# Kernel tuning notes

Measured on AMD Instinct MI355X. Metric: run time of the kernel, lower is better.

## Reference

```python
import jax, jax.numpy as jnp
import numpy as np

N, D, C = 4096, 512, 64
MARGIN = 1.0
INF = jnp.float32(1e30)


def setup_inputs() -> dict:
    key = jax.random.key(0)
    k1, k2 = jax.random.split(key)
    embeddings = jax.random.normal(k1, (N, D), dtype=jnp.float32)
    targets = jax.random.randint(k2, (N,), 0, C)
    return {"embeddings": embeddings, "targets": targets}


def _triplet_loss(embeddings, targets, margin=MARGIN):
    # Squared pairwise distances [N, N] (differentiable, used for the loss)
    sq_norms = jnp.sum(embeddings * embeddings, axis=1)
    sq_dist = jnp.maximum(
        sq_norms[:, None] + sq_norms[None, :] - 2.0 * (embeddings @ embeddings.T), 0.0
    )
    # Euclidean distances for mining only (index selection is non-differentiable in torch)
    dist = jnp.sqrt(jax.lax.stop_gradient(sq_dist))

    same = targets[:, None] == targets[None, :]  # [N, N] same-label mask

    # Hardest negative per anchor: argmax_k (d_ap - d_ak + margin) == argmin_k d_ak over negatives
    neg_dist = jnp.where(same, INF, dist)
    n_idx = jnp.argmin(neg_dist, axis=1)   # [N] hardest negative index per anchor
    min_neg = jnp.min(neg_dist, axis=1)    # [N] its euclidean distance

    idx = jnp.arange(dist.shape[0])
    # anchor-positive pairs: same label, a < p (torch.combinations on sorted indices)
    pair_mask = same & (idx[:, None] < idx[None, :])
    # triplet kept only if mined loss (euclidean) strictly positive
    valid = pair_mask & (dist - min_neg[:, None] + margin > 0)

    ap_sq = sq_dist                         # [N, N] squared anchor-positive distances
    an_sq = sq_dist[idx, n_idx]             # [N]   squared anchor-hard-negative distances
    losses = jax.nn.relu(ap_sq - an_sq[:, None] + margin)

    cnt = jnp.sum(valid)
    denom = jnp.maximum(cnt, 1).astype(losses.dtype)
    loss = jnp.sum(jnp.where(valid, losses, 0.0)) / denom

    correct = jnp.sum(valid & (ap_sq < an_sq[:, None]))
    accuracy = correct.astype(jnp.float32) / jnp.maximum(cnt, 1).astype(jnp.float32)
    return loss, accuracy


def reference(embeddings, targets):
    return _triplet_loss(embeddings, targets)
```

## Files before the change

kernel.cpp:

```cpp
#include <hip/hip_runtime.h>

#define N 4096
#define D 512
#define C 64
#define MARGIN 1.0f
#define TILE 64
#define ROWB 128
#define NTILES (N / TILE)
#define NTRI (NTILES * (NTILES + 1) / 2)
#define FINF 3.0e38f
#define SLOTW 16
#define PCAP 512
#define LOSSB 128

typedef __attribute__((ext_vector_type(8))) short short8;
typedef __attribute__((ext_vector_type(4))) float floatx4;

__device__ __forceinline__ unsigned short f2bf(float f) {
  unsigned int u = __float_as_uint(f);
  u += 0x7FFFu + ((u >> 16) & 1u);
  return (unsigned short)(u >> 16);
}

__device__ __forceinline__ void gload_lds16(const void* g, void* l) {
  __builtin_amdgcn_global_load_lds(
      (const __attribute__((address_space(1))) unsigned int*)g,
      (__attribute__((address_space(3))) unsigned int*)l, 16, 0, 0);
}

__global__ __launch_bounds__(256) void prep_kernel(const float* __restrict__ E,
                                                   unsigned short* __restrict__ Ebf,
                                                   float* __restrict__ norms,
                                                   unsigned int* __restrict__ an_sq_bits,
                                                   unsigned int* __restrict__ accs_u,
                                                   unsigned int* __restrict__ ctrl) {
  const int row = blockIdx.x;
  const int tid = threadIdx.x;
  if (row == N) {
    for (int k = tid; k < C * SLOTW; k += 256) accs_u[k] = 0u;
    if (tid < 2) ctrl[tid] = 0u;
    return;
  }
  if (row < 16) an_sq_bits[row * 256 + tid] = 0x7F800000u;
  const float2 v = reinterpret_cast<const float2*>(E + (size_t)row * D)[tid];
  float s = v.x * v.x + v.y * v.y;
  unsigned int packed = ((unsigned int)f2bf(v.y) << 16) | (unsigned int)f2bf(v.x);
  reinterpret_cast<unsigned int*>(Ebf + (size_t)row * D)[tid] = packed;
  for (int off = 32; off > 0; off >>= 1) s += __shfl_down(s, off);
  __shared__ float wsum[4];
  if ((tid & 63) == 0) wsum[tid >> 6] = s;
  __syncthreads();
  if (tid == 0) norms[row] = wsum[0] + wsum[1] + wsum[2] + wsum[3];
}

__global__ __launch_bounds__(256, 4) void gemm_min_kernel(const unsigned short* __restrict__ Ebf,
                                                          const float* __restrict__ norms,
                                                          const int* __restrict__ targets,
                                                          unsigned int* __restrict__ an_sq_bits,
                                                          uint2* __restrict__ pairs,
                                                          unsigned int* __restrict__ ctrl) {
  const int u = (blockIdx.x & 7) * (NTRI / 8) + (blockIdx.x >> 3);
  int i = (int)((sqrtf(8.0f * (float)u + 1.0f) - 1.0f) * 0.5f);
  while ((i + 1) * (i + 2) / 2 <= u) ++i;
  while (i * (i + 1) / 2 > u) --i;
  const int tm = u - i * (i + 1) / 2;
  const int tn = i;

  __shared__ alignas(16) unsigned char As[TILE * ROWB];
  __shared__ alignas(16) unsigned char Bs[TILE * ROWB];
  __shared__ float s_rmin[2][TILE];
  __shared__ float s_cmin[2][TILE];
  __shared__ unsigned int s_pkey[PCAP];
  __shared__ float s_psq[PCAP];
  __shared__ unsigned int s_pcnt, s_pbase;

  const int tid = threadIdx.x;
  const int wave = tid >> 6, lane = tid & 63;
  const int quad = lane >> 4, l16 = lane & 15;
  const int wr = wave >> 1, wc = wave & 1;
  const int rowBase = tm * TILE, colBase = tn * TILE;
  if (tid == 0) s_pcnt = 0u;

  const int lr = lane >> 3;
  const int lq = (lane & 7) ^ lr;
  const int lofs = lr * (D * 2) + lq * 16;
  const unsigned char* gA = (const unsigned char*)Ebf + (size_t)rowBase * (D * 2);
  const unsigned char* gB = (const unsigned char*)Ebf + (size_t)colBase * (D * 2);

  const int swz = l16 & 7;
  int rA[2], rB[2], cq[2];
#pragma unroll
  for (int s = 0; s < 2; s++) {
    rA[s] = (wr * 32 + s * 16 + l16) * ROWB;
    rB[s] = (wc * 32 + s * 16 + l16) * ROWB;
  }
#pragma unroll
  for (int ks = 0; ks < 2; ks++) cq[ks] = ((ks * 4 + quad) ^ swz) * 16;

  floatx4 acc[2][2];
#pragma unroll
  for (int a = 0; a < 2; a++)
#pragma unroll
    for (int b = 0; b < 2; b++) acc[a][b] = (floatx4){0.f, 0.f, 0.f, 0.f};

  for (int k0b = 0; k0b < D * 2; k0b += 128) {
#pragma unroll
    for (int t = 0; t < 2; t++) {
      const int g = wave * 2 + t;
      gload_lds16(gA + (size_t)g * 8 * (D * 2) + lofs + k0b, As + g * 1024);
      gload_lds16(gB + (size_t)g * 8 * (D * 2) + lofs + k0b, Bs + g * 1024);
    }
    __syncthreads();
#pragma unroll
    for (int ks = 0; ks < 2; ks++) {
      short8 af[2], bf[2];
#pragma unroll
      for (int s = 0; s < 2; s++) {
        af[s] = *reinterpret_cast<const short8*>(As + rA[s] + cq[ks]);
        bf[s] = *reinterpret_cast<const short8*>(Bs + rB[s] + cq[ks]);
      }
#pragma unroll
      for (int sm = 0; sm < 2; sm++)
#pragma unroll
        for (int sn = 0; sn < 2; sn++)
          acc[sm][sn] = __builtin_amdgcn_mfma_f32_16x16x32_bf16(af[sm], bf[sn], acc[sm][sn], 0, 0, 0);
    }
    __syncthreads();
  }

  int tcol[2], gcolv[2];
  float ncol[2];
#pragma unroll
  for (int sn = 0; sn < 2; sn++) {
    const int gc = colBase + wc * 32 + sn * 16 + l16;
    gcolv[sn] = gc;
    tcol[sn] = targets[gc];
    ncol[sn] = norms[gc];
  }
  float colmin[2] = {FINF, FINF};
#pragma unroll
  for (int sm = 0; sm < 2; sm++) {
#pragma unroll
    for (int r = 0; r < 4; r++) {
      const int rloc = wr * 32 + sm * 16 + quad * 4 + r;
      const int grow = rowBase + rloc;
      const int trow = targets[grow];
      const float nrow = norms[grow];
      float rowmin = FINF;
#pragma unroll
      for (int sn = 0; sn < 2; sn++) {
        const float sq = fmaxf(nrow + ncol[sn] - 2.0f * acc[sm][sn][r], 0.0f);
        if (tcol[sn] != trow) {
          rowmin = fminf(rowmin, sq);
          colmin[sn] = fminf(colmin[sn], sq);
        } else if (grow < gcolv[sn]) {
          const unsigned int idx = atomicAdd(&s_pcnt, 1u);
          if (idx < PCAP) {
            s_pkey[idx] = ((unsigned int)grow << 12) | (unsigned int)gcolv[sn];
            s_psq[idx] = sq;
          } else {
            const unsigned int g = atomicAdd(&ctrl[0], 1u);
            pairs[g] = make_uint2(((unsigned int)grow << 12) | (unsigned int)gcolv[sn],
                                  __float_as_uint(sq));
          }
        }
      }
#pragma unroll
      for (int off = 1; off < 16; off <<= 1) rowmin = fminf(rowmin, __shfl_xor(rowmin, off));
      if (l16 == 0) s_rmin[wc][rloc] = rowmin;
    }
  }
#pragma unroll
  for (int sn = 0; sn < 2; sn++) {
    float cm = colmin[sn];
    cm = fminf(cm, __shfl_xor(cm, 16));
    cm = fminf(cm, __shfl_xor(cm, 32));
    if (quad == 0) s_cmin[wr][wc * 32 + sn * 16 + l16] = cm;
  }
  __syncthreads();
  if (tid < TILE) {
    const float m = fminf(s_rmin[0][tid], s_rmin[1][tid]);
    if (m < FINF) atomicMin(&an_sq_bits[rowBase + tid], __float_as_uint(m));
  } else if (tid < 2 * TILE) {
    const int c = tid - TILE;
    const float m = fminf(s_cmin[0][c], s_cmin[1][c]);
    if (m < FINF) atomicMin(&an_sq_bits[colBase + c], __float_as_uint(m));
  }
  const unsigned int npair = min(s_pcnt, (unsigned int)PCAP);
  if (tid == 0) s_pbase = atomicAdd(&ctrl[0], npair);
  __syncthreads();
  for (unsigned int r = tid; r < npair; r += 256)
    pairs[s_pbase + r] = make_uint2(s_pkey[r], __float_as_uint(s_psq[r]));
}

__global__ __launch_bounds__(256) void loss_kernel(const uint2* __restrict__ pairs,
                                                   const unsigned int* __restrict__ an_sq_bits,
                                                   float* __restrict__ accs,
                                                   unsigned int* __restrict__ ctrl,
                                                   float* __restrict__ out) {
  const int tid = threadIdx.x, wave = tid >> 6, lane = tid & 63;
  const unsigned int M = ctrl[0];
  __shared__ float s_sum[4];
  __shared__ unsigned int s_cnt[4], s_cor[4];
  __shared__ int s_last;
  float bsum = 0.f;
  unsigned int bcnt = 0, bcor = 0;
  for (unsigned int r = blockIdx.x * 256 + tid; r < M; r += LOSSB * 256) {
    const uint2 rec = pairs[r];
    const int a = (int)(rec.x >> 12);
    const float sq = __uint_as_float(rec.y);
    const float an = __uint_as_float(an_sq_bits[a]);
    if (sqrtf(sq) - sqrtf(an) + MARGIN > 0.0f) {
      bcnt++;
      bsum += fmaxf(sq - an + MARGIN, 0.0f);
      if (sq < an) bcor++;
    }
  }
#pragma unroll
  for (int off = 32; off > 0; off >>= 1) {
    bsum += __shfl_down(bsum, off);
    bcnt += __shfl_down(bcnt, off);
    bcor += __shfl_down(bcor, off);
  }
  if (lane == 0) { s_sum[wave] = bsum; s_cnt[wave] = bcnt; s_cor[wave] = bcor; }
  __syncthreads();
  if (tid == 0) {
    float* slot = accs + (size_t)(blockIdx.x & (C - 1)) * SLOTW;
    atomicAdd(&slot[0], s_sum[0] + s_sum[1] + s_sum[2] + s_sum[3]);
    atomicAdd((unsigned int*)&slot[1], s_cnt[0] + s_cnt[1] + s_cnt[2] + s_cnt[3]);
    atomicAdd((unsigned int*)&slot[2], s_cor[0] + s_cor[1] + s_cor[2] + s_cor[3]);
    __threadfence();
    s_last = (atomicAdd(&ctrl[1], 1u) == (unsigned int)LOSSB - 1u);
  }
  __syncthreads();
  if (s_last) {
    __threadfence();
    if (tid < C) {
      float sum = __uint_as_float(atomicAdd((unsigned int*)&accs[(size_t)tid * SLOTW + 0], 0u));
      unsigned int cnt = atomicAdd((unsigned int*)&accs[(size_t)tid * SLOTW + 1], 0u);
      unsigned int cor = atomicAdd((unsigned int*)&accs[(size_t)tid * SLOTW + 2], 0u);
#pragma unroll
      for (int off = 32; off > 0; off >>= 1) {
        sum += __shfl_down(sum, off);
        cnt += __shfl_down(cnt, off);
        cor += __shfl_down(cor, off);
      }
      if (tid == 0) {
        const float denom = (float)(cnt > 0u ? cnt : 1u);
        out[0] = sum / denom;
        out[1] = (float)cor / denom;
      }
    }
  }
}

extern "C" void kernel_launch(void* const* d_in, const int* in_sizes, int n_in,
                              void* d_out, int out_size, void* d_ws, size_t ws_size,
                              hipStream_t stream) {
  const float* E = (const float*)d_in[0];
  const int* targets = (const int*)d_in[1];
  float* out = (float*)d_out;
  char* ws = (char*)d_ws;
  size_t off = 0;
  unsigned short* Ebf = (unsigned short*)(ws + off); off += (size_t)N * D * 2;
  float* norms = (float*)(ws + off); off += (size_t)N * 4;
  unsigned int* an_sq = (unsigned int*)(ws + off); off += (size_t)N * 4;
  float* accs = (float*)(ws + off); off += (size_t)C * SLOTW * 4;
  unsigned int* ctrl = (unsigned int*)(ws + off); off += 256;
  uint2* pairs = (uint2*)(ws + off);

  prep_kernel<<<dim3(N + 1), dim3(256), 0, stream>>>(E, Ebf, norms, an_sq, (unsigned int*)accs, ctrl);
  gemm_min_kernel<<<dim3(NTRI), dim3(256), 0, stream>>>(Ebf, norms, targets, an_sq, pairs, ctrl);
  loss_kernel<<<dim3(LOSSB), dim3(256), 0, stream>>>(pairs, an_sq, accs, ctrl, out);
}
```

Baseline: 110.1 us.

## Pre-layout bf16 embeddings in MFMA fragment order and load operands directly from global

The prep kernel now writes the bf16 embeddings in a blocked layout matching the 16x16x32 MFMA operand fragment order, with 16-row groups and 1KB chunks along K. The GEMM kernel drops the LDS staging buffers, the global-to-LDS loads and both barriers, and has each wave read its fragments straight from global memory with 16-byte loads. This removes LDS traffic and synchronisation and frees shared memory. The cost is that A and B tiles are no longer shared through LDS within a block, so each wave fetches them again and relies on L1/L2 hits.

Result: slower. 121.0 us (+9.9%).

```diff
diff --git a/kernel.cpp b/kernel.cpp
--- a/kernel.cpp
+++ b/kernel.cpp
@@ -5,7 +5,6 @@
 #define C 64
 #define MARGIN 1.0f
 #define TILE 64
-#define ROWB 128
 #define NTILES (N / TILE)
 #define NTRI (NTILES * (NTILES + 1) / 2)
 #define FINF 3.0e38f
@@ -22,14 +21,8 @@
   return (unsigned short)(u >> 16);
 }
 
-__device__ __forceinline__ void gload_lds16(const void* g, void* l) {
-  __builtin_amdgcn_global_load_lds(
-      (const __attribute__((address_space(1))) unsigned int*)g,
-      (__attribute__((address_space(3))) unsigned int*)l, 16, 0, 0);
-}
-
 __global__ __launch_bounds__(256) void prep_kernel(const float* __restrict__ E,
-                                                   unsigned short* __restrict__ Ebf,
+                                                   unsigned int* __restrict__ Ebt,
                                                    float* __restrict__ norms,
                                                    unsigned int* __restrict__ an_sq_bits,
                                                    unsigned int* __restrict__ accs_u,
@@ -45,7 +38,7 @@
   const float2 v = reinterpret_cast<const float2*>(E + (size_t)row * D)[tid];
   float s = v.x * v.x + v.y * v.y;
   unsigned int packed = ((unsigned int)f2bf(v.y) << 16) | (unsigned int)f2bf(v.x);
-  reinterpret_cast<unsigned int*>(Ebf + (size_t)row * D)[tid] = packed;
+  Ebt[((size_t)(row >> 4) << 12) + ((tid >> 4) << 8) + ((row & 15) << 4) + (tid & 15)] = packed;
   for (int off = 32; off > 0; off >>= 1) s += __shfl_down(s, off);
   __shared__ float wsum[4];
   if ((tid & 63) == 0) wsum[tid >> 6] = s;
@@ -53,7 +46,7 @@
   if (tid == 0) norms[row] = wsum[0] + wsum[1] + wsum[2] + wsum[3];
 }
 
-__global__ __launch_bounds__(256, 4) void gemm_min_kernel(const unsigned short* __restrict__ Ebf,
+__global__ __launch_bounds__(256, 4) void gemm_min_kernel(const unsigned int* __restrict__ Ebt,
                                                           const float* __restrict__ norms,
                                                           const int* __restrict__ targets,
                                                           unsigned int* __restrict__ an_sq_bits,
@@ -66,8 +59,6 @@
   const int tm = u - i * (i + 1) / 2;
   const int tn = i;
 
-  __shared__ alignas(16) unsigned char As[TILE * ROWB];
-  __shared__ alignas(16) unsigned char Bs[TILE * ROWB];
   __shared__ float s_rmin[2][TILE];
   __shared__ float s_cmin[2][TILE];
   __shared__ unsigned int s_pkey[PCAP];
@@ -81,21 +72,15 @@
   const int rowBase = tm * TILE, colBase = tn * TILE;
   if (tid == 0) s_pcnt = 0u;
 
-  const int lr = lane >> 3;
-  const int lq = (lane & 7) ^ lr;
-  const int lofs = lr * (D * 2) + lq * 16;
-  const unsigned char* gA = (const unsigned char*)Ebf + (size_t)rowBase * (D * 2);
-  const unsigned char* gB = (const unsigned char*)Ebf + (size_t)colBase * (D * 2);
-
-  const int swz = l16 & 7;
-  int rA[2], rB[2], cq[2];
+  const unsigned char* Eb = (const unsigned char*)Ebt;
+  const int lbyte = l16 * 64 + quad * 16;
+  const unsigned char* pA[2];
+  const unsigned char* pB[2];
 #pragma unroll
   for (int s = 0; s < 2; s++) {
-    rA[s] = (wr * 32 + s * 16 + l16) * ROWB;
-    rB[s] = (wc * 32 + s * 16 + l16) * ROWB;
-  }
-#pragma unroll
-  for (int ks = 0; ks < 2; ks++) cq[ks] = ((ks * 4 + quad) ^ swz) * 16;
+    pA[s] = Eb + ((size_t)(tm * 4 + wr * 2 + s) << 14) + lbyte;
+    pB[s] = Eb + ((size_t)(tn * 4 + wc * 2 + s) << 14) + lbyte;
+  }
 
   floatx4 acc[2][2];
 #pragma unroll
@@ -103,29 +88,19 @@
 #pragma unroll
     for (int b = 0; b < 2; b++) acc[a][b] = (floatx4){0.f, 0.f, 0.f, 0.f};
 
-  for (int k0b = 0; k0b < D * 2; k0b += 128) {
-#pragma unroll
-    for (int t = 0; t < 2; t++) {
-      const int g = wave * 2 + t;
-      gload_lds16(gA + (size_t)g * 8 * (D * 2) + lofs + k0b, As + g * 1024);
-      gload_lds16(gB + (size_t)g * 8 * (D * 2) + lofs + k0b, Bs + g * 1024);
-    }
-    __syncthreads();
-#pragma unroll
-    for (int ks = 0; ks < 2; ks++) {
-      short8 af[2], bf[2];
-#pragma unroll
-      for (int s = 0; s < 2; s++) {
-        af[s] = *reinterpret_cast<const short8*>(As + rA[s] + cq[ks]);
-        bf[s] = *reinterpret_cast<const short8*>(Bs + rB[s] + cq[ks]);
-      }
-#pragma unroll
-      for (int sm = 0; sm < 2; sm++)
-#pragma unroll
-        for (int sn = 0; sn < 2; sn++)
-          acc[sm][sn] = __builtin_amdgcn_mfma_f32_16x16x32_bf16(af[sm], bf[sn], acc[sm][sn], 0, 0, 0);
-    }
-    __syncthreads();
+#pragma unroll
+  for (int c = 0; c < 16; ++c) {
+    short8 af[2], bf[2];
+#pragma unroll
+    for (int s = 0; s < 2; s++) {
+      af[s] = *reinterpret_cast<const short8*>(pA[s] + c * 1024);
+      bf[s] = *reinterpret_cast<const short8*>(pB[s] + c * 1024);
+    }
+#pragma unroll
+    for (int sm = 0; sm < 2; sm++)
+#pragma unroll
+      for (int sn = 0; sn < 2; sn++)
+        acc[sm][sn] = __builtin_amdgcn_mfma_f32_16x16x32_bf16(af[sm], bf[sn], acc[sm][sn], 0, 0, 0);
   }
 
   int tcol[2], gcolv[2];
@@ -262,14 +237,14 @@
   float* out = (float*)d_out;
   char* ws = (char*)d_ws;
   size_t off = 0;
-  unsigned short* Ebf = (unsigned short*)(ws + off); off += (size_t)N * D * 2;
+  unsigned int* Ebt = (unsigned int*)(ws + off); off += (size_t)N * D * 2;
   float* norms = (float*)(ws + off); off += (size_t)N * 4;
   unsigned int* an_sq = (unsigned int*)(ws + off); off += (size_t)N * 4;
   float* accs = (float*)(ws + off); off += (size_t)C * SLOTW * 4;
   unsigned int* ctrl = (unsigned int*)(ws + off); off += 256;
   uint2* pairs = (uint2*)(ws + off);
 
-  prep_kernel<<<dim3(N + 1), dim3(256), 0, stream>>>(E, Ebf, norms, an_sq, (unsigned int*)accs, ctrl);
-  gemm_min_kernel<<<dim3(NTRI), dim3(256), 0, stream>>>(Ebf, norms, targets, an_sq, pairs, ctrl);
+  prep_kernel<<<dim3(N + 1), dim3(256), 0, stream>>>(E, Ebt, norms, an_sq, (unsigned int*)accs, ctrl);
+  gemm_min_kernel<<<dim3(NTRI), dim3(256), 0, stream>>>(Ebt, norms, targets, an_sq, pairs, ctrl);
   loss_kernel<<<dim3(LOSSB), dim3(256), 0, stream>>>(pairs, an_sq, accs, ctrl, out);
 }
```
